# Optimization experiments

Measured on AMD Instinct MI355X. Metric: run time of the kernel, lower is better.

## Reference

```python
import jax, jax.numpy as jnp
import numpy as np

B, N, FIN, FOUT, E = 2, 50000, 128, 64, 800000


def setup_inputs() -> dict:
    key = jax.random.key(0)
    ks = jax.random.split(key, 7)
    x = jax.random.normal(ks[0], (B, N, FIN), dtype=jnp.float32)
    W = jax.random.normal(ks[1], (FIN, FOUT), dtype=jnp.float32) * (1.0 / np.sqrt(FIN))
    W_self = jax.random.normal(ks[2], (FIN, FOUT), dtype=jnp.float32) * (1.0 / np.sqrt(FIN))
    b_self = jax.random.normal(ks[3], (FOUT,), dtype=jnp.float32) * 0.01
    edge_row = jax.random.randint(ks[4], (E,), 0, N, dtype=jnp.int32)
    edge_col = jax.random.randint(ks[5], (E,), 0, N, dtype=jnp.int32)
    edge_val = jax.random.uniform(ks[6], (E,), dtype=jnp.float32)
    return {"x": x, "W": W, "W_self": W_self, "b_self": b_self,
            "edge_row": edge_row, "edge_col": edge_col, "edge_val": edge_val}


def reference(x, W, W_self, b_self, edge_row, edge_col, edge_val):
    # x: (B, N, FIN); adjacency in COO form: out[r] += val * in[c]
    Bn, Nn, _ = x.shape
    Fo = W.shape[1]
    x_trans = jnp.einsum("bnf,fo->bno", x, W)               # (B, N, FOUT), no bias
    # Same layout trick as torch: sparse.mm over (N, B*FOUT)
    xr = x_trans.transpose(1, 0, 2).reshape(Nn, Bn * Fo)    # (N, B*FOUT)
    msgs = edge_val[:, None] * xr[edge_col]                  # (E, B*FOUT) gather
    agg = jax.ops.segment_sum(msgs, edge_row, num_segments=Nn)  # (N, B*FOUT) scatter-add
    agg = agg.reshape(Nn, Bn, Fo).transpose(1, 0, 2)         # (B, N, FOUT)
    self_c = jnp.einsum("bnf,fo->bno", x, W_self) + b_self   # Linear with bias
    return jax.nn.relu(self_c + agg)
```

## Files before the change

### kernel.cpp

```cpp
#include <hip/hip_runtime.h>
#include <hip/hip_fp16.h>

#define Bc   2
#define Nn   50000
#define FINc 128
#define FOUTc 64
#define Mtot (Bc * Nn)
#define CCOMB 128
#define GB 1563
#define CB 782

typedef __bf16 bf16x8 __attribute__((ext_vector_type(8)));
typedef float  f32x4  __attribute__((ext_vector_type(4)));

static __device__ inline unsigned short f2bf(float f) {
    unsigned int u = __float_as_uint(f);
    u += 0x7fffu + ((u >> 16) & 1u);
    return (unsigned short)(u >> 16);
}

__global__ __launch_bounds__(256) void pack_w(
    const float* __restrict__ W, const float* __restrict__ Ws,
    unsigned short* __restrict__ Bp)
{
    const int idx = blockIdx.x * 256 + threadIdx.x;
    const int lane = idx & 63;
    const int kt   = (idx >> 6) & 3;
    const int nt   = idx >> 8;
    const int n    = nt * 16 + (lane & 15);
    const int k0   = kt * 32 + (lane >> 4) * 8;
    unsigned short o8[8];
#pragma unroll
    for (int j = 0; j < 8; ++j) {
        const int f = k0 + j;
        const float v = (n < 64) ? W[f * FOUTc + n] : Ws[f * FOUTc + (n - 64)];
        o8[j] = f2bf(v);
    }
    *(uint4*)&Bp[(size_t)idx * 8] = *(uint4*)o8;
}

__global__ __launch_bounds__(256) void gemm_count(
    const float* __restrict__ x, const unsigned short* __restrict__ Bp,
    const float* __restrict__ bself,
    unsigned short* __restrict__ xrb, float* __restrict__ outp,
    const int* __restrict__ erow, int* __restrict__ cntp,
    int* __restrict__ rank, int E)
{
    if (blockIdx.x >= GB) {
        const int base = (blockIdx.x - GB) * 1024 + threadIdx.x * 4;
        if (base + 4 <= E) {
            const int4 r4 = *(const int4*)&erow[base];
            const int k0 = atomicAdd(&cntp[(size_t)r4.x * 16], 1);
            const int k1 = atomicAdd(&cntp[(size_t)r4.y * 16], 1);
            const int k2 = atomicAdd(&cntp[(size_t)r4.z * 16], 1);
            const int k3 = atomicAdd(&cntp[(size_t)r4.w * 16], 1);
            *(int4*)&rank[base] = make_int4(k0, k1, k2, k3);
        }
        return;
    }

    const int wave = threadIdx.x >> 6;
    const int lane = threadIdx.x & 63;
    const int quad = lane >> 4;
    const int mbase = blockIdx.x * 64 + wave * 16;

    const int mrow   = mbase + (lane & 15);
    const int mclamp = (mrow < Mtot) ? mrow : (Mtot - 1);
    const float* __restrict__ xrow = &x[(size_t)mclamp * FINc];

    f32x4 acc[8] = {};

#pragma unroll
    for (int kt = 0; kt < 4; ++kt) {
        const int k0 = kt * 32 + quad * 8;
        const float4 xa = *(const float4*)&xrow[k0];
        const float4 xb = *(const float4*)&xrow[k0 + 4];
        bf16x8 bf;
        bf[0] = (__bf16)xa.x; bf[1] = (__bf16)xa.y;
        bf[2] = (__bf16)xa.z; bf[3] = (__bf16)xa.w;
        bf[4] = (__bf16)xb.x; bf[5] = (__bf16)xb.y;
        bf[6] = (__bf16)xb.z; bf[7] = (__bf16)xb.w;

        const bf16x8* __restrict__ abase =
            (const bf16x8*)&Bp[(size_t)(kt * 64 + lane) * 8];
#pragma unroll
        for (int nt = 0; nt < 8; ++nt) {
            const bf16x8 af = abase[nt * 4 * 64];
            acc[nt] = __builtin_amdgcn_mfma_f32_16x16x32_bf16(af, bf, acc[nt], 0, 0, 0);
        }
    }

    const int m = mbase + (lane & 15);
    if (m < Mtot) {
        const int b = (m >= Nn) ? 1 : 0;
        const int n = m - b * Nn;
        unsigned short* __restrict__ xp = &xrb[(size_t)n * CCOMB + b * FOUTc];
        const int cq = quad * 4;
#pragma unroll
        for (int nt = 0; nt < 4; ++nt) {
            const int c = nt * 16 + cq;
            unsigned short h[4];
            h[0] = f2bf(acc[nt][0]); h[1] = f2bf(acc[nt][1]);
            h[2] = f2bf(acc[nt][2]); h[3] = f2bf(acc[nt][3]);
            *(uint2*)&xp[c] = *(uint2*)h;
        }
        float* __restrict__ op = &outp[(size_t)m * FOUTc];
#pragma unroll
        for (int nt = 4; nt < 8; ++nt) {
            const int o = (nt - 4) * 16 + cq;
            const float4 b4 = *(const float4*)&bself[o];
            float4 v;
            v.x = acc[nt][0] + b4.x; v.y = acc[nt][1] + b4.y;
            v.z = acc[nt][2] + b4.z; v.w = acc[nt][3] + b4.w;
            *(float4*)&op[o] = v;
        }
    }
}

__global__ __launch_bounds__(256) void block_sum(
    const int* __restrict__ cntp, int* __restrict__ bsum)
{
    __shared__ int s[256];
    const int t = threadIdx.x;
    const int idx = blockIdx.x * 256 + t;
    s[t] = (idx < Nn) ? cntp[(size_t)idx * 16] : 0;
    __syncthreads();
    for (int off = 128; off > 0; off >>= 1) {
        if (t < off) s[t] += s[t + off];
        __syncthreads();
    }
    if (t == 0) bsum[blockIdx.x] = s[0];
}

__global__ __launch_bounds__(256) void scan_bsum(
    const int* __restrict__ bsum, int* __restrict__ bscan, int nb)
{
    __shared__ int s[256];
    const int t = threadIdx.x;
    const int v = (t < nb) ? bsum[t] : 0;
    s[t] = v;
    __syncthreads();
    for (int off = 1; off < 256; off <<= 1) {
        const int add = (t >= off) ? s[t - off] : 0;
        __syncthreads();
        s[t] += add;
        __syncthreads();
    }
    if (t < nb) bscan[t] = s[t] - v;
}

__global__ __launch_bounds__(256) void fill_starts(
    const int* __restrict__ cntp, const int* __restrict__ bscan,
    int* __restrict__ rowstart, int E)
{
    __shared__ int s[256];
    const int t = threadIdx.x;
    const int idx = blockIdx.x * 256 + t;
    const int v = (idx < Nn) ? cntp[(size_t)idx * 16] : 0;
    s[t] = v;
    __syncthreads();
    for (int off = 1; off < 256; off <<= 1) {
        const int add = (t >= off) ? s[t - off] : 0;
        __syncthreads();
        s[t] += add;
        __syncthreads();
    }
    if (idx < Nn) rowstart[idx] = bscan[blockIdx.x] + (s[t] - v);
    if (idx == 0) rowstart[Nn] = E;
}

__global__ __launch_bounds__(256) void bucket(
    const int* __restrict__ erow, const int* __restrict__ ecol,
    const float* __restrict__ evalv, const int* __restrict__ rank,
    const int* __restrict__ rowstart, unsigned int* __restrict__ cvp, int E)
{
    const int e = blockIdx.x * 512 + threadIdx.x * 2;
    if (e + 2 > E) return;
    const int2   r2 = *(const int2*)&erow[e];
    const int2   c2 = *(const int2*)&ecol[e];
    const float2 v2 = *(const float2*)&evalv[e];
    const int2   k2 = *(const int2*)&rank[e];
    const unsigned int h0 = __half_as_ushort(__float2half(v2.x));
    const unsigned int h1 = __half_as_ushort(__float2half(v2.y));
    cvp[rowstart[r2.x] + k2.x] = (h0 << 17) | (unsigned int)c2.x;
    cvp[rowstart[r2.y] + k2.y] = (h1 << 17) | (unsigned int)c2.y;
}

#define GATH16(EIDX, ACC)                                                     \
    {                                                                         \
        const unsigned int w = cvp[EIDX];                                     \
        const float vv = __half2float(__ushort_as_half(                       \
                             (unsigned short)(w >> 17)));                     \
        const uint4 raw = *(const uint4*)&xrb[(size_t)(w & 0x1FFFFu) * CCOMB + c0]; \
        ACC[0] = fmaf(vv, __uint_as_float(raw.x << 16),         ACC[0]);      \
        ACC[1] = fmaf(vv, __uint_as_float(raw.x & 0xffff0000u), ACC[1]);      \
        ACC[2] = fmaf(vv, __uint_as_float(raw.y << 16),         ACC[2]);      \
        ACC[3] = fmaf(vv, __uint_as_float(raw.y & 0xffff0000u), ACC[3]);      \
        ACC[4] = fmaf(vv, __uint_as_float(raw.z << 16),         ACC[4]);      \
        ACC[5] = fmaf(vv, __uint_as_float(raw.z & 0xffff0000u), ACC[5]);      \
        ACC[6] = fmaf(vv, __uint_as_float(raw.w << 16),         ACC[6]);      \
        ACC[7] = fmaf(vv, __uint_as_float(raw.w & 0xffff0000u), ACC[7]);      \
    }

__global__ __launch_bounds__(256) void row_gather(
    const int* __restrict__ rowstart, const unsigned int* __restrict__ cvp,
    const unsigned short* __restrict__ xrb, float* __restrict__ outp)
{
    const int lane = threadIdx.x & 63;
    int n = blockIdx.x * 4 + (threadIdx.x >> 6);
    n = __builtin_amdgcn_readfirstlane(n);

    const int s    = rowstart[n];
    const int eend = rowstart[n + 1];
    const int sub  = lane >> 4;
    const int c0   = (lane & 15) * 8;

    float aA[8] = {0.f, 0.f, 0.f, 0.f, 0.f, 0.f, 0.f, 0.f};
    float aB[8] = {0.f, 0.f, 0.f, 0.f, 0.f, 0.f, 0.f, 0.f};

    int e = s;
    for (; e + 8 <= eend; e += 8) {
        GATH16(e + sub,     aA);
        GATH16(e + 4 + sub, aB);
    }
    for (; e < eend; e += 4) {
        if (e + sub < eend) GATH16(e + sub, aA);
    }

#pragma unroll
    for (int i = 0; i < 8; ++i) {
        aA[i] += aB[i];
        aA[i] += __shfl_down(aA[i], 16);
        aA[i] += __shfl_down(aA[i], 32);
    }

    if (lane < 16) {
        const int b = c0 >> 6;
        const int o = c0 & 63;
        const size_t oidx = ((size_t)b * Nn + n) * FOUTc + o;
        float4 s0 = *(float4*)&outp[oidx];
        float4 s1 = *(float4*)&outp[oidx + 4];
        s0.x = fmaxf(s0.x + aA[0], 0.0f);
        s0.y = fmaxf(s0.y + aA[1], 0.0f);
        s0.z = fmaxf(s0.z + aA[2], 0.0f);
        s0.w = fmaxf(s0.w + aA[3], 0.0f);
        s1.x = fmaxf(s1.x + aA[4], 0.0f);
        s1.y = fmaxf(s1.y + aA[5], 0.0f);
        s1.z = fmaxf(s1.z + aA[6], 0.0f);
        s1.w = fmaxf(s1.w + aA[7], 0.0f);
        *(float4*)&outp[oidx]     = s0;
        *(float4*)&outp[oidx + 4] = s1;
    }
}

extern "C" void kernel_launch(void* const* d_in, const int* in_sizes, int n_in,
                              void* d_out, int out_size, void* d_ws, size_t ws_size,
                              hipStream_t stream)
{
    const float* x    = (const float*)d_in[0];
    const float* W    = (const float*)d_in[1];
    const float* Ws   = (const float*)d_in[2];
    const float* bs   = (const float*)d_in[3];
    const int*   erow = (const int*)d_in[4];
    const int*   ecol = (const int*)d_in[5];
    const float* eval = (const float*)d_in[6];
    float* outp = (float*)d_out;
    const int E = in_sizes[4];

    unsigned short* xrb = (unsigned short*)d_ws;
    unsigned int* cvp = (unsigned int*)(xrb + (size_t)Nn * CCOMB);
    int* rank     = (int*)(cvp + E);
    int* rowstart = rank + E;
    int* cntp     = rowstart + (Nn + 4);
    int* bsum     = cntp + (size_t)Nn * 16;
    int* bscan    = bsum + 256;
    unsigned short* Bp = (unsigned short*)(bscan + 256);

    const int NB = (Nn + 255) / 256;

    hipMemsetAsync(cntp, 0, (size_t)Nn * 16 * sizeof(int), stream);
    pack_w<<<8, 256, 0, stream>>>(W, Ws, Bp);

    gemm_count<<<GB + CB, 256, 0, stream>>>(x, Bp, bs, xrb, outp,
                                            erow, cntp, rank, E);

    block_sum<<<NB, 256, 0, stream>>>(cntp, bsum);
    scan_bsum<<<1, 256, 0, stream>>>(bsum, bscan, NB);
    fill_starts<<<NB, 256, 0, stream>>>(cntp, bscan, rowstart, E);

    bucket<<<(E + 511) / 512, 256, 0, stream>>>(erow, ecol, eval, rank,
                                                rowstart, cvp, E);

    row_gather<<<Nn / 4, 256, 0, stream>>>(rowstart, cvp, xrb, outp);
}
```

Baseline: 209.0 us.

## Restructure GCN pipeline: fused prep, decoupled-lookback scan, bf16 self term, split-batch gather

The memset and weight packing are merged into one prep kernel, and edge counting is split out of the GEMM into its own kernel. The three-kernel scan becomes a single kernel that publishes per-block totals and has each block spin-wait on the flags of earlier blocks. The self-linear result is stored as bf16 in a workspace buffer instead of fp32 in the output, and the row gather now splits the two batches across blocks with 8 edges per step, reading that bf16 buffer and writing the final output once. Together these aim to cut launch count and fp32 read-modify-write traffic, at the cost of bf16 rounding of the self term and a scan that relies on all earlier blocks being resident.

```diff
diff --git a/kernel.cpp b/kernel.cpp
--- a/kernel.cpp
+++ b/kernel.cpp
@@ -8,7 +8,9 @@
 #define Mtot (Bc * Nn)
 #define CCOMB 128
 #define GB 1563
-#define CB 782
+#define EB4 782
+#define NB 196
+#define ZTOT (Nn * 16 + 256)
 
 typedef __bf16 bf16x8 __attribute__((ext_vector_type(8)));
 typedef float  f32x4  __attribute__((ext_vector_type(4)));
@@ -19,50 +21,54 @@
     return (unsigned short)(u >> 16);
 }
 
-__global__ __launch_bounds__(256) void pack_w(
+__global__ __launch_bounds__(256) void prep(
     const float* __restrict__ W, const float* __restrict__ Ws,
-    unsigned short* __restrict__ Bp)
-{
-    const int idx = blockIdx.x * 256 + threadIdx.x;
-    const int lane = idx & 63;
-    const int kt   = (idx >> 6) & 3;
-    const int nt   = idx >> 8;
-    const int n    = nt * 16 + (lane & 15);
-    const int k0   = kt * 32 + (lane >> 4) * 8;
-    unsigned short o8[8];
-#pragma unroll
-    for (int j = 0; j < 8; ++j) {
-        const int f = k0 + j;
-        const float v = (n < 64) ? W[f * FOUTc + n] : Ws[f * FOUTc + (n - 64)];
-        o8[j] = f2bf(v);
-    }
-    *(uint4*)&Bp[(size_t)idx * 8] = *(uint4*)o8;
-}
-
-__global__ __launch_bounds__(256) void gemm_count(
+    unsigned short* __restrict__ Bp, int* __restrict__ zbase)
+{
+    if (blockIdx.x < 8) {
+        const int idx = blockIdx.x * 256 + threadIdx.x;
+        const int lane = idx & 63;
+        const int kt   = (idx >> 6) & 3;
+        const int nt   = idx >> 8;
+        const int n    = nt * 16 + (lane & 15);
+        const int k0   = kt * 32 + (lane >> 4) * 8;
+        unsigned short o8[8];
+#pragma unroll
+        for (int j = 0; j < 8; ++j) {
+            const int f = k0 + j;
+            const float v = (n < 64) ? W[f * FOUTc + n] : Ws[f * FOUTc + (n - 64)];
+            o8[j] = f2bf(v);
+        }
+        *(uint4*)&Bp[(size_t)idx * 8] = *(uint4*)o8;
+    } else {
+        const int i4 = (blockIdx.x - 8) * 1024 + threadIdx.x * 4;
+        if (i4 + 4 <= ZTOT)
+            *(int4*)&zbase[i4] = make_int4(0, 0, 0, 0);
+    }
+}
+
+__global__ __launch_bounds__(256) void count_edges(
+    const int* __restrict__ erow, int* __restrict__ cntp,
+    int* __restrict__ rank, int E)
+{
+    const int base = blockIdx.x * 1024 + threadIdx.x * 4;
+    if (base + 4 > E) return;
+    const int4 r4 = *(const int4*)&erow[base];
+    const int k0 = atomicAdd(&cntp[(size_t)r4.x * 16], 1);
+    const int k1 = atomicAdd(&cntp[(size_t)r4.y * 16], 1);
+    const int k2 = atomicAdd(&cntp[(size_t)r4.z * 16], 1);
+    const int k3 = atomicAdd(&cntp[(size_t)r4.w * 16], 1);
+    *(int4*)&rank[base] = make_int4(k0, k1, k2, k3);
+}
+
+__global__ __launch_bounds__(256) void gemm_mfma(
     const float* __restrict__ x, const unsigned short* __restrict__ Bp,
     const float* __restrict__ bself,
-    unsigned short* __restrict__ xrb, float* __restrict__ outp,
-    const int* __restrict__ erow, int* __restrict__ cntp,
-    int* __restrict__ rank, int E)
-{
-    if (blockIdx.x >= GB) {
-        const int base = (blockIdx.x - GB) * 1024 + threadIdx.x * 4;
-        if (base + 4 <= E) {
-            const int4 r4 = *(const int4*)&erow[base];
-            const int k0 = atomicAdd(&cntp[(size_t)r4.x * 16], 1);
-            const int k1 = atomicAdd(&cntp[(size_t)r4.y * 16], 1);
-            const int k2 = atomicAdd(&cntp[(size_t)r4.z * 16], 1);
-            const int k3 = atomicAdd(&cntp[(size_t)r4.w * 16], 1);
-            *(int4*)&rank[base] = make_int4(k0, k1, k2, k3);
-        }
-        return;
-    }
-
-    const int wave = threadIdx.x >> 6;
+    unsigned short* __restrict__ xrb, unsigned short* __restrict__ selfb)
+{
     const int lane = threadIdx.x & 63;
     const int quad = lane >> 4;
-    const int mbase = blockIdx.x * 64 + wave * 16;
+    const int mbase = blockIdx.x * 64 + (threadIdx.x >> 6) * 16;
 
     const int mrow   = mbase + (lane & 15);
     const int mclamp = (mrow < Mtot) ? mrow : (Mtot - 1);
@@ -104,40 +110,28 @@
             h[2] = f2bf(acc[nt][2]); h[3] = f2bf(acc[nt][3]);
             *(uint2*)&xp[c] = *(uint2*)h;
         }
-        float* __restrict__ op = &outp[(size_t)m * FOUTc];
+        unsigned short* __restrict__ sp = &selfb[(size_t)m * FOUTc];
 #pragma unroll
         for (int nt = 4; nt < 8; ++nt) {
             const int o = (nt - 4) * 16 + cq;
             const float4 b4 = *(const float4*)&bself[o];
-            float4 v;
-            v.x = acc[nt][0] + b4.x; v.y = acc[nt][1] + b4.y;
-            v.z = acc[nt][2] + b4.z; v.w = acc[nt][3] + b4.w;
-            *(float4*)&op[o] = v;
-        }
-    }
-}
-
-__global__ __launch_bounds__(256) void block_sum(
-    const int* __restrict__ cntp, int* __restrict__ bsum)
+            unsigned short h[4];
+            h[0] = f2bf(acc[nt][0] + b4.x); h[1] = f2bf(acc[nt][1] + b4.y);
+            h[2] = f2bf(acc[nt][2] + b4.z); h[3] = f2bf(acc[nt][3] + b4.w);
+            *(uint2*)&sp[o] = *(uint2*)h;
+        }
+    }
+}
+
+__global__ __launch_bounds__(256) void scan_fill(
+    const int* __restrict__ cntp, int* __restrict__ aggf,
+    int* __restrict__ rowstart, int E)
 {
     __shared__ int s[256];
-    const int t = threadIdx.x;
-    const int idx = blockIdx.x * 256 + t;
-    s[t] = (idx < Nn) ? cntp[(size_t)idx * 16] : 0;
-    __syncthreads();
-    for (int off = 128; off > 0; off >>= 1) {
-        if (t < off) s[t] += s[t + off];
-        __syncthreads();
-    }
-    if (t == 0) bsum[blockIdx.x] = s[0];
-}
-
-__global__ __launch_bounds__(256) void scan_bsum(
-    const int* __restrict__ bsum, int* __restrict__ bscan, int nb)
-{
-    __shared__ int s[256];
-    const int t = threadIdx.x;
-    const int v = (t < nb) ? bsum[t] : 0;
+    const int t = threadIdx.x, b = blockIdx.x;
+    const int idx = b * 256 + t;
+    const int v = (idx < Nn) ? cntp[(size_t)idx * 16] : 0;
+
     s[t] = v;
     __syncthreads();
     for (int off = 1; off < 256; off <<= 1) {
@@ -146,27 +140,28 @@
         s[t] += add;
         __syncthreads();
     }
-    if (t < nb) bscan[t] = s[t] - v;
-}
-
-__global__ __launch_bounds__(256) void fill_starts(
-    const int* __restrict__ cntp, const int* __restrict__ bscan,
-    int* __restrict__ rowstart, int E)
-{
-    __shared__ int s[256];
-    const int t = threadIdx.x;
-    const int idx = blockIdx.x * 256 + t;
-    const int v = (idx < Nn) ? cntp[(size_t)idx * 16] : 0;
-    s[t] = v;
+    const int excl  = s[t] - v;
+    const int total = s[255];
+
+    if (t == 0) atomicOr(&aggf[b], (total << 1) | 1);
+
+    int a = 0;
+    if (t < b) {
+        int w;
+        do { w = atomicOr(&aggf[t], 0); } while (!(w & 1));
+        a = w >> 1;
+    }
     __syncthreads();
-    for (int off = 1; off < 256; off <<= 1) {
-        const int add = (t >= off) ? s[t - off] : 0;
+    s[t] = a;
+    __syncthreads();
+    for (int off = 128; off > 0; off >>= 1) {
+        if (t < off) s[t] += s[t + off];
         __syncthreads();
-        s[t] += add;
-        __syncthreads();
-    }
-    if (idx < Nn) rowstart[idx] = bscan[blockIdx.x] + (s[t] - v);
-    if (idx == 0) rowstart[Nn] = E;
+    }
+    const int pre = s[0];
+
+    if (idx < Nn) rowstart[idx] = pre + excl;
+    if (b == 0 && t == 0) rowstart[Nn] = E;
 }
 
 __global__ __launch_bounds__(256) void bucket(
@@ -174,19 +169,23 @@
     const float* __restrict__ evalv, const int* __restrict__ rank,
     const int* __restrict__ rowstart, unsigned int* __restrict__ cvp, int E)
 {
-    const int e = blockIdx.x * 512 + threadIdx.x * 2;
-    if (e + 2 > E) return;
-    const int2   r2 = *(const int2*)&erow[e];
-    const int2   c2 = *(const int2*)&ecol[e];
-    const float2 v2 = *(const float2*)&evalv[e];
-    const int2   k2 = *(const int2*)&rank[e];
-    const unsigned int h0 = __half_as_ushort(__float2half(v2.x));
-    const unsigned int h1 = __half_as_ushort(__float2half(v2.y));
-    cvp[rowstart[r2.x] + k2.x] = (h0 << 17) | (unsigned int)c2.x;
-    cvp[rowstart[r2.y] + k2.y] = (h1 << 17) | (unsigned int)c2.y;
-}
-
-#define GATH16(EIDX, ACC)                                                     \
+    const int base = blockIdx.x * 1024 + threadIdx.x * 4;
+    if (base + 4 > E) return;
+    const int4   r4 = *(const int4*)&erow[base];
+    const int4   c4 = *(const int4*)&ecol[base];
+    const float4 v4 = *(const float4*)&evalv[base];
+    const int4   k4 = *(const int4*)&rank[base];
+    cvp[rowstart[r4.x] + k4.x] =
+        ((unsigned int)__half_as_ushort(__float2half(v4.x)) << 17) | (unsigned int)c4.x;
+    cvp[rowstart[r4.y] + k4.y] =
+        ((unsigned int)__half_as_ushort(__float2half(v4.y)) << 17) | (unsigned int)c4.y;
+    cvp[rowstart[r4.z] + k4.z] =
+        ((unsigned int)__half_as_ushort(__float2half(v4.z)) << 17) | (unsigned int)c4.z;
+    cvp[rowstart[r4.w] + k4.w] =
+        ((unsigned int)__half_as_ushort(__float2half(v4.w)) << 17) | (unsigned int)c4.w;
+}
+
+#define GATH8(EIDX, ACC)                                                      \
     {                                                                         \
         const unsigned int w = cvp[EIDX];                                     \
         const float vv = __half2float(__ushort_as_half(                       \
@@ -204,52 +203,62 @@
 
 __global__ __launch_bounds__(256) void row_gather(
     const int* __restrict__ rowstart, const unsigned int* __restrict__ cvp,
-    const unsigned short* __restrict__ xrb, float* __restrict__ outp)
-{
+    const unsigned short* __restrict__ xrb, const unsigned short* __restrict__ selfb,
+    float* __restrict__ outp)
+{
+    const int j    = blockIdx.x;
+    const int low3 = j & 7;
+    const int h    = (low3 >= 4) ? 1 : 0;
+    const int ord  = (j >> 3) * 4 + (low3 & 3);
+    int n = ord * 4 + (threadIdx.x >> 6);
+    n = __builtin_amdgcn_readfirstlane(n);
+
     const int lane = threadIdx.x & 63;
-    int n = blockIdx.x * 4 + (threadIdx.x >> 6);
-    n = __builtin_amdgcn_readfirstlane(n);
+    const int slot = lane >> 3;
+    const int c0   = h * 64 + (lane & 7) * 8;
 
     const int s    = rowstart[n];
     const int eend = rowstart[n + 1];
-    const int sub  = lane >> 4;
-    const int c0   = (lane & 15) * 8;
 
     float aA[8] = {0.f, 0.f, 0.f, 0.f, 0.f, 0.f, 0.f, 0.f};
     float aB[8] = {0.f, 0.f, 0.f, 0.f, 0.f, 0.f, 0.f, 0.f};
 
     int e = s;
-    for (; e + 8 <= eend; e += 8) {
-        GATH16(e + sub,     aA);
-        GATH16(e + 4 + sub, aB);
-    }
-    for (; e < eend; e += 4) {
-        if (e + sub < eend) GATH16(e + sub, aA);
-    }
+    for (; e + 16 <= eend; e += 16) {
+        GATH8(e + slot,     aA);
+        GATH8(e + 8 + slot, aB);
+    }
+    if (e + 8 <= eend) {
+        GATH8(e + slot, aA);
+        e += 8;
+    }
+    if (e + slot < eend) GATH8(e + slot, aB);
 
 #pragma unroll
     for (int i = 0; i < 8; ++i) {
         aA[i] += aB[i];
+        aA[i] += __shfl_down(aA[i], 8);
         aA[i] += __shfl_down(aA[i], 16);
         aA[i] += __shfl_down(aA[i], 32);
     }
 
-    if (lane < 16) {
-        const int b = c0 >> 6;
-        const int o = c0 & 63;
-        const size_t oidx = ((size_t)b * Nn + n) * FOUTc + o;
-        float4 s0 = *(float4*)&outp[oidx];
-        float4 s1 = *(float4*)&outp[oidx + 4];
-        s0.x = fmaxf(s0.x + aA[0], 0.0f);
-        s0.y = fmaxf(s0.y + aA[1], 0.0f);
-        s0.z = fmaxf(s0.z + aA[2], 0.0f);
-        s0.w = fmaxf(s0.w + aA[3], 0.0f);
-        s1.x = fmaxf(s1.x + aA[4], 0.0f);
-        s1.y = fmaxf(s1.y + aA[5], 0.0f);
-        s1.z = fmaxf(s1.z + aA[6], 0.0f);
-        s1.w = fmaxf(s1.w + aA[7], 0.0f);
-        *(float4*)&outp[oidx]     = s0;
-        *(float4*)&outp[oidx + 4] = s1;
+    if (lane < 8) {
+        const size_t m = (size_t)h * Nn + n;
+        const int o = lane * 8;
+        const uint4 sb = *(const uint4*)&selfb[m * FOUTc + o];
+        float sv[8];
+        sv[0] = __uint_as_float(sb.x << 16); sv[1] = __uint_as_float(sb.x & 0xffff0000u);
+        sv[2] = __uint_as_float(sb.y << 16); sv[3] = __uint_as_float(sb.y & 0xffff0000u);
+        sv[4] = __uint_as_float(sb.z << 16); sv[5] = __uint_as_float(sb.z & 0xffff0000u);
+        sv[6] = __uint_as_float(sb.w << 16); sv[7] = __uint_as_float(sb.w & 0xffff0000u);
+        float4 s0, s1;
+        s0.x = fmaxf(sv[0] + aA[0], 0.0f); s0.y = fmaxf(sv[1] + aA[1], 0.0f);
+        s0.z = fmaxf(sv[2] + aA[2], 0.0f); s0.w = fmaxf(sv[3] + aA[3], 0.0f);
+        s1.x = fmaxf(sv[4] + aA[4], 0.0f); s1.y = fmaxf(sv[5] + aA[5], 0.0f);
+        s1.z = fmaxf(sv[6] + aA[6], 0.0f); s1.w = fmaxf(sv[7] + aA[7], 0.0f);
+        float* __restrict__ op = &outp[m * FOUTc + o];
+        *(float4*)&op[0] = s0;
+        *(float4*)&op[4] = s1;
     }
 }
 
@@ -267,29 +276,24 @@
     float* outp = (float*)d_out;
     const int E = in_sizes[4];
 
-    unsigned short* xrb = (unsigned short*)d_ws;
-    unsigned int* cvp = (unsigned int*)(xrb + (size_t)Nn * CCOMB);
+    unsigned short* xrb   = (unsigned short*)d_ws;
+    unsigned short* selfb = xrb + (size_t)Nn * CCOMB;
+    unsigned int*   cvp   = (unsigned int*)(selfb + (size_t)Mtot * FOUTc);
     int* rank     = (int*)(cvp + E);
     int* rowstart = rank + E;
-    int* cntp     = rowstart + (Nn + 4);
-    int* bsum     = cntp + (size_t)Nn * 16;
-    int* bscan    = bsum + 256;
-    unsigned short* Bp = (unsigned short*)(bscan + 256);
-
-    const int NB = (Nn + 255) / 256;
-
-    hipMemsetAsync(cntp, 0, (size_t)Nn * 16 * sizeof(int), stream);
-    pack_w<<<8, 256, 0, stream>>>(W, Ws, Bp);
-
-    gemm_count<<<GB + CB, 256, 0, stream>>>(x, Bp, bs, xrb, outp,
-                                            erow, cntp, rank, E);
-
-    block_sum<<<NB, 256, 0, stream>>>(cntp, bsum);
-    scan_bsum<<<1, 256, 0, stream>>>(bsum, bscan, NB);
-    fill_starts<<<NB, 256, 0, stream>>>(cntp, bscan, rowstart, E);
-
-    bucket<<<(E + 511) / 512, 256, 0, stream>>>(erow, ecol, eval, rank,
-                                                rowstart, cvp, E);
-
-    row_gather<<<Nn / 4, 256, 0, stream>>>(rowstart, cvp, xrb, outp);
-}
+    int* cntp     = rowstart + (Nn + 8);
+    int* aggf     = cntp + (size_t)Nn * 16;
+    unsigned short* Bp = (unsigned short*)(aggf + 256);
+
+    prep<<<8 + (ZTOT + 1023) / 1024, 256, 0, stream>>>(W, Ws, Bp, cntp);
+
+    count_edges<<<EB4, 256, 0, stream>>>(erow, cntp, rank, E);
+
+    gemm_mfma<<<GB, 256, 0, stream>>>(x, Bp, bs, xrb, selfb);
+
+    scan_fill<<<NB, 256, 0, stream>>>(cntp, aggf, rowstart, E);
+
+    bucket<<<EB4, 256, 0, stream>>>(erow, ecol, eval, rank, rowstart, cvp, E);
+
+    row_gather<<<Nn / 2, 256, 0, stream>>>(rowstart, cvp, xrb, selfb, outp);
+}
```

Result: slower. 213.4 us (+2.1%).
